# Performance work log

Measured on AMD Instinct MI355X. Metric: run time of the kernel, lower is better.

The kernel has to match this reference:

```python
import jax, jax.numpy as jnp
import numpy as np

B, P, T = 4096, 16, 8
IN_DIM, OUT_DIM, K = 128, 128, 2
N_TABLE = 100000


def setup_inputs() -> dict:
    key = jax.random.key(0)
    ks = jax.random.split(key, 8)
    return {
        "path_input": jax.random.randint(ks[0], (B, P, T), 0, N_TABLE, dtype=jnp.int32),
        "path_num": P,
        "timestamp": T,
        "path_type": jax.random.randint(ks[1], (T,), 0, 4, dtype=jnp.int32),
        "user_emb": jax.random.normal(ks[2], (N_TABLE, IN_DIM), jnp.float32),
        "item_emb": jax.random.normal(ks[3], (N_TABLE, IN_DIM), jnp.float32),
        "ca_emb": jax.random.normal(ks[4], (N_TABLE, IN_DIM), jnp.float32),
        "ci_emb": jax.random.normal(ks[5], (N_TABLE, IN_DIM), jnp.float32),
        "conv_w": jax.random.normal(ks[6], (OUT_DIM, IN_DIM, K), jnp.float32) * 0.05,
        "conv_b": jax.random.normal(ks[7], (OUT_DIM,), jnp.float32) * 0.05,
    }


def reference(path_input, path_num, timestamp, path_type,
              user_emb, item_emb, ca_emb, ci_emb, conv_w, conv_b):
    b, p, t = path_input.shape
    # [4, N, D] stacked tables; per-position table selection via path_type
    tables = jnp.stack([user_emb, item_emb, ca_emb, ci_emb])
    # emb: [B, P, T, D]  (advanced indexing: path_type broadcasts over B, P)
    emb = tables[path_type[None, None, :], path_input]
    # conv1d over time: [B*P, D, T] -> [B*P, out, T-K+1]
    x = emb.reshape(b * p, t, -1).transpose(0, 2, 1)
    y = jax.lax.conv_general_dilated(
        x, conv_w, window_strides=(1,), padding='VALID',
        dimension_numbers=('NCH', 'OIH', 'NCH')) + conv_b[None, :, None]
    # max-pool over time, then over paths (dropout is identity in eval)
    y = y.max(axis=-1).reshape(b, p, -1)  # [B, P, out]
    return y.max(axis=1)  # [B, out]
```

## Files before the change

### kernel.cpp

```cpp
#include <hip/hip_runtime.h>

#define NB   4096
#define NBLK 256
#define NJ   16

typedef __attribute__((ext_vector_type(4))) float f32x4;
typedef __attribute__((ext_vector_type(8))) short short8;
typedef __attribute__((ext_vector_type(4))) int   int4v;
typedef __attribute__((ext_vector_type(2))) int   int2v;

union Frag { int4v i; short8 s; };

__device__ __forceinline__ unsigned short f2bf(float f) {
  unsigned int u = __float_as_uint(f);
  u = (u + 0x7FFFu + ((u >> 16) & 1u)) >> 16;
  return (unsigned short)u;
}

__device__ __forceinline__ int cvtpk(float lo, float hi) {
  int r;
  asm("v_cvt_pk_bf16_f32 %0, %1, %2" : "=v"(r) : "v"(lo), "v"(hi));
  return r;
}

__global__ __launch_bounds__(512)
void wconv_kernel(const float* __restrict__ conv_w, unsigned short* __restrict__ ws)
{
  int flat = blockIdx.x * 512 + threadIdx.x;
  int lane = flat & 63;
  int ng   = (flat >> 6) & 7;
  int ker  = (flat >> 9) & 1;
  int kk   = flat >> 10;
  int col  = ng * 16 + (lane & 15);
  int k0   = kk * 32 + (lane >> 4) * 8;
  short8 s;
#pragma unroll
  for (int j = 0; j < 8; ++j)
    s[j] = (short)f2bf(conv_w[col * 256 + (k0 + j) * 2 + ker]);
  *(short8*)(ws + (size_t)flat * 8) = s;
}

#define RED_OFF 35088
#define LDS_BYTES 36112
#define A_STRIDE 272

__global__ __launch_bounds__(512)
void path_emb_kernel(const int* __restrict__ path_input,
                     const int* __restrict__ path_type,
                     const float* __restrict__ t0, const float* __restrict__ t1,
                     const float* __restrict__ t2, const float* __restrict__ t3,
                     const unsigned short* __restrict__ wfrag,
                     const float* __restrict__ conv_b,
                     float* __restrict__ out)
{
  __shared__ __align__(16) char lds[LDS_BYTES];
  const int blk  = blockIdx.x;
  const int tid  = threadIdx.x;
  const int wid  = tid >> 6;
  const int lane = tid & 63;
  const int lrow = lane & 15;
  const int lk   = lane >> 4;
  const int R = wid & 1;
  const int C = wid >> 1;

  const int* idxg = path_input + (size_t)blk * NJ * 128;
  float cb = (tid < 128) ? conv_b[tid] : 0.0f;

  const int grow = tid >> 2;
  const int gq   = tid & 3;
  const int ty   = path_type[grow & 7];
  const float* tb = (ty == 0) ? t0 : (ty == 1) ? t1 : (ty == 2) ? t2 : t3;

  Frag wreg[4][2][2];
#pragma unroll
  for (int kk = 0; kk < 4; ++kk)
#pragma unroll
    for (int ker = 0; ker < 2; ++ker)
#pragma unroll
      for (int n = 0; n < 2; ++n) {
        int f = (kk * 2 + ker) * 8 + C * 2 + n;
        wreg[kk][ker][n].i = *(const int4v*)(wfrag + (size_t)f * 512 + lane * 8);
      }

  auto ISSUE = [&](int j, f32x4 (&ld)[8]) {
    int idx = idxg[j * 128 + grow];
    const float* g = tb + (size_t)idx * 128 + gq * 4;
#pragma unroll
    for (int i = 0; i < 8; ++i) ld[i] = *(const f32x4*)(g + i * 16);
  };
  auto WRITE = [&](const f32x4 (&ld)[8]) {
    char* dst = lds + grow * A_STRIDE + gq * 8;
#pragma unroll
    for (int i = 0; i < 8; ++i) {
      int2v w;
      w[0] = cvtpk(ld[i][0], ld[i][1]);
      w[1] = cvtpk(ld[i][2], ld[i][3]);
      *(int2v*)(dst + i * 32) = w;
    }
  };

  float* red = (float*)(lds + RED_OFF);
  const int arow0 = R * 64 + lrow;

  auto COMPUTE = [&]() {
    f32x4 acc[4][2] = {};
#pragma unroll
    for (int kk = 0; kk < 4; ++kk) {
      Frag alo[4], ahi[4];
#pragma unroll
      for (int m = 0; m < 4; ++m) {
        const char* p = lds + (arow0 + m * 16) * A_STRIDE + kk * 64 + lk * 16;
        alo[m].i = *(const int4v*)(p);
        ahi[m].i = *(const int4v*)(p + A_STRIDE);
      }
#pragma unroll
      for (int m = 0; m < 4; ++m)
#pragma unroll
        for (int n = 0; n < 2; ++n) {
          acc[m][n] = __builtin_amdgcn_mfma_f32_16x16x32_bf16(
              alo[m].s, wreg[kk][0][n].s, acc[m][n], 0, 0, 0);
          acc[m][n] = __builtin_amdgcn_mfma_f32_16x16x32_bf16(
              ahi[m].s, wreg[kk][1][n].s, acc[m][n], 0, 0, 0);
        }
    }
    float vmax[2] = {-1e30f, -1e30f};
#pragma unroll
    for (int m = 0; m < 4; ++m)
#pragma unroll
      for (int n = 0; n < 2; ++n)
#pragma unroll
        for (int r = 0; r < 4; ++r) {
          int rloc = lk * 4 + r;
          if ((rloc & 7) == 7) continue;
          vmax[n] = fmaxf(vmax[n], acc[m][n][r]);
        }
#pragma unroll
    for (int n = 0; n < 2; ++n) {
      float v = vmax[n];
      v = fmaxf(v, __shfl_xor(v, 16));
      v = fmaxf(v, __shfl_xor(v, 32));
      vmax[n] = v;
    }
    if (lane < 16) {
#pragma unroll
      for (int n = 0; n < 2; ++n)
        red[R * 128 + C * 32 + n * 16 + lane] = vmax[n];
    }
  };

  auto BAR = [&]() {
    asm volatile("s_waitcnt lgkmcnt(0)" ::: "memory");
    __builtin_amdgcn_sched_barrier(0);
    __builtin_amdgcn_s_barrier();
    __builtin_amdgcn_sched_barrier(0);
  };

  f32x4 lA[8], lB[8], lC[8];
  ISSUE(0, lA);
  ISSUE(1, lB);
  ISSUE(2, lC);
  WRITE(lA);
  BAR();

#pragma unroll
  for (int j = 0; j < NJ; ++j) {
    if (j + 3 < NJ) {
      if (j % 3 == 0)      ISSUE(j + 3, lA);
      else if (j % 3 == 1) ISSUE(j + 3, lB);
      else                 ISSUE(j + 3, lC);
    }
    __builtin_amdgcn_sched_barrier(0);

    COMPUTE();
    BAR();

    if (tid < 128)
      out[(size_t)(blk * NJ + j) * 128 + tid] =
          fmaxf(red[tid], red[128 + tid]) + cb;

    if (j + 1 < NJ) {
      if ((j + 1) % 3 == 0)      WRITE(lA);
      else if ((j + 1) % 3 == 1) WRITE(lB);
      else                       WRITE(lC);
    }
    BAR();
  }
}

extern "C" void kernel_launch(void* const* d_in, const int* in_sizes, int n_in,
                              void* d_out, int out_size, void* d_ws, size_t ws_size,
                              hipStream_t stream) {
  const int*   path_input = (const int*)d_in[0];
  const int*   path_type  = (const int*)d_in[3];
  const float* user_emb   = (const float*)d_in[4];
  const float* item_emb   = (const float*)d_in[5];
  const float* ca_emb     = (const float*)d_in[6];
  const float* ci_emb     = (const float*)d_in[7];
  const float* conv_w     = (const float*)d_in[8];
  const float* conv_b     = (const float*)d_in[9];
  float* out = (float*)d_out;
  unsigned short* wfrag = (unsigned short*)d_ws;

  wconv_kernel<<<dim3(8), dim3(512), 0, stream>>>(conv_w, wfrag);
  path_emb_kernel<<<dim3(NBLK), dim3(512), 0, stream>>>(
      path_input, path_type, user_emb, item_emb, ca_emb, ci_emb,
      wfrag, conv_b, out);
}
```

Baseline: 53.89 us.

## Split work into many small blocks with double-buffered LDS and no cross-wave reduction

```diff
diff --git a/kernel.cpp b/kernel.cpp
--- a/kernel.cpp
+++ b/kernel.cpp
@@ -1,8 +1,6 @@
 #include <hip/hip_runtime.h>
 
-#define NB   4096
-#define NBLK 256
-#define NJ   16
+#define NBLK 2048
 
 typedef __attribute__((ext_vector_type(4))) float f32x4;
 typedef __attribute__((ext_vector_type(8))) short short8;
@@ -40,11 +38,11 @@
   *(short8*)(ws + (size_t)flat * 8) = s;
 }
 
-#define RED_OFF 35088
-#define LDS_BYTES 36112
 #define A_STRIDE 272
+#define ABUF     (65 * A_STRIDE)
+#define LDS_BYTES (2 * ABUF)
 
-__global__ __launch_bounds__(512)
+__global__ __launch_bounds__(256)
 void path_emb_kernel(const int* __restrict__ path_input,
                      const int* __restrict__ path_type,
                      const float* __restrict__ t0, const float* __restrict__ t1,
@@ -56,20 +54,26 @@
   __shared__ __align__(16) char lds[LDS_BYTES];
   const int blk  = blockIdx.x;
   const int tid  = threadIdx.x;
-  const int wid  = tid >> 6;
+  const int C    = tid >> 6;
   const int lane = tid & 63;
   const int lrow = lane & 15;
-  const int lk   = lane >> 4;
-  const int R = wid & 1;
-  const int C = wid >> 1;
-
-  const int* idxg = path_input + (size_t)blk * NJ * 128;
-  float cb = (tid < 128) ? conv_b[tid] : 0.0f;
+  const int g    = lane >> 4;
 
   const int grow = tid >> 2;
   const int gq   = tid & 3;
+  {
+  }
   const int ty   = path_type[grow & 7];
   const float* tb = (ty == 0) ? t0 : (ty == 1) ? t1 : (ty == 2) ? t2 : t3;
+
+  int idx[4];
+#pragma unroll
+  for (int jb = 0; jb < 4; ++jb)
+    idx[jb] = path_input[((size_t)blk * 2 + (jb >> 1)) * 128 + (jb & 1) * 64 + grow];
+
+  float cb[2];
+#pragma unroll
+  for (int n = 0; n < 2; ++n) cb[n] = conv_b[C * 32 + n * 16 + lrow];
 
   Frag wreg[4][2][2];
 #pragma unroll
@@ -82,14 +86,14 @@
         wreg[kk][ker][n].i = *(const int4v*)(wfrag + (size_t)f * 512 + lane * 8);
       }
 
-  auto ISSUE = [&](int j, f32x4 (&ld)[8]) {
-    int idx = idxg[j * 128 + grow];
-    const float* g = tb + (size_t)idx * 128 + gq * 4;
+  f32x4 ld[8];
+  auto ISSUE = [&](int jb) {
+    const float* base = tb + (size_t)idx[jb] * 128 + gq * 4;
 #pragma unroll
-    for (int i = 0; i < 8; ++i) ld[i] = *(const f32x4*)(g + i * 16);
+    for (int i = 0; i < 8; ++i) ld[i] = *(const f32x4*)(base + i * 16);
   };
-  auto WRITE = [&](const f32x4 (&ld)[8]) {
-    char* dst = lds + grow * A_STRIDE + gq * 8;
+  auto WRITE = [&](int buf) {
+    char* dst = lds + buf * ABUF + grow * A_STRIDE + gq * 8;
 #pragma unroll
     for (int i = 0; i < 8; ++i) {
       int2v w;
@@ -99,52 +103,32 @@
     }
   };
 
-  float* red = (float*)(lds + RED_OFF);
-  const int arow0 = R * 64 + lrow;
+  float vmax[2] = {-1e30f, -1e30f};
 
-  auto COMPUTE = [&]() {
-    f32x4 acc[4][2] = {};
+  auto COMPUTE = [&](int buf) {
+    const char* Ab = lds + buf * ABUF;
 #pragma unroll
-    for (int kk = 0; kk < 4; ++kk) {
-      Frag alo[4], ahi[4];
+    for (int m = 0; m < 4; ++m) {
+      f32x4 acc[2] = {};
 #pragma unroll
-      for (int m = 0; m < 4; ++m) {
-        const char* p = lds + (arow0 + m * 16) * A_STRIDE + kk * 64 + lk * 16;
-        alo[m].i = *(const int4v*)(p);
-        ahi[m].i = *(const int4v*)(p + A_STRIDE);
+      for (int kk = 0; kk < 4; ++kk) {
+        Frag alo, ahi;
+        const char* p = Ab + (m * 16 + lrow) * A_STRIDE + kk * 64 + g * 16;
+        alo.i = *(const int4v*)(p);
+        ahi.i = *(const int4v*)(p + A_STRIDE);
+        acc[0] = __builtin_amdgcn_mfma_f32_16x16x32_bf16(alo.s, wreg[kk][0][0].s, acc[0], 0, 0, 0);
+        acc[1] = __builtin_amdgcn_mfma_f32_16x16x32_bf16(alo.s, wreg[kk][0][1].s, acc[1], 0, 0, 0);
+        acc[0] = __builtin_amdgcn_mfma_f32_16x16x32_bf16(ahi.s, wreg[kk][1][0].s, acc[0], 0, 0, 0);
+        acc[1] = __builtin_amdgcn_mfma_f32_16x16x32_bf16(ahi.s, wreg[kk][1][1].s, acc[1], 0, 0, 0);
       }
-#pragma unroll
-      for (int m = 0; m < 4; ++m)
-#pragma unroll
-        for (int n = 0; n < 2; ++n) {
-          acc[m][n] = __builtin_amdgcn_mfma_f32_16x16x32_bf16(
-              alo[m].s, wreg[kk][0][n].s, acc[m][n], 0, 0, 0);
-          acc[m][n] = __builtin_amdgcn_mfma_f32_16x16x32_bf16(
-              ahi[m].s, wreg[kk][1][n].s, acc[m][n], 0, 0, 0);
-        }
-    }
-    float vmax[2] = {-1e30f, -1e30f};
-#pragma unroll
-    for (int m = 0; m < 4; ++m)
 #pragma unroll
       for (int n = 0; n < 2; ++n)
 #pragma unroll
         for (int r = 0; r < 4; ++r) {
-          int rloc = lk * 4 + r;
+          int rloc = g * 4 + r;
           if ((rloc & 7) == 7) continue;
-          vmax[n] = fmaxf(vmax[n], acc[m][n][r]);
+          vmax[n] = fmaxf(vmax[n], acc[n][r]);
         }
-#pragma unroll
-    for (int n = 0; n < 2; ++n) {
-      float v = vmax[n];
-      v = fmaxf(v, __shfl_xor(v, 16));
-      v = fmaxf(v, __shfl_xor(v, 32));
-      vmax[n] = v;
-    }
-    if (lane < 16) {
-#pragma unroll
-      for (int n = 0; n < 2; ++n)
-        red[R * 128 + C * 32 + n * 16 + lane] = vmax[n];
     }
   };
 
@@ -155,34 +139,35 @@
     __builtin_amdgcn_sched_barrier(0);
   };
 
-  f32x4 lA[8], lB[8], lC[8];
-  ISSUE(0, lA);
-  ISSUE(1, lB);
-  ISSUE(2, lC);
-  WRITE(lA);
+  ISSUE(0);
+  WRITE(0);
   BAR();
 
 #pragma unroll
-  for (int j = 0; j < NJ; ++j) {
-    if (j + 3 < NJ) {
-      if (j % 3 == 0)      ISSUE(j + 3, lA);
-      else if (j % 3 == 1) ISSUE(j + 3, lB);
-      else                 ISSUE(j + 3, lC);
-    }
+  for (int jb = 0; jb < 4; ++jb) {
+    if (jb + 1 < 4) ISSUE(jb + 1);
     __builtin_amdgcn_sched_barrier(0);
 
-    COMPUTE();
-    BAR();
+    COMPUTE(jb & 1);
 
-    if (tid < 128)
-      out[(size_t)(blk * NJ + j) * 128 + tid] =
-          fmaxf(red[tid], red[128 + tid]) + cb;
+    if (jb & 1) {
+#pragma unroll
+      for (int n = 0; n < 2; ++n) {
+        float v = vmax[n];
+        v = fmaxf(v, __shfl_xor(v, 16));
+        v = fmaxf(v, __shfl_xor(v, 32));
+        vmax[n] = v;
+      }
+      if (lane < 16) {
+        int b = blk * 2 + (jb >> 1);
+#pragma unroll
+        for (int n = 0; n < 2; ++n)
+          out[(size_t)b * 128 + C * 32 + n * 16 + lrow] = vmax[n] + cb[n];
+      }
+      vmax[0] = -1e30f; vmax[1] = -1e30f;
+    }
 
-    if (j + 1 < NJ) {
-      if ((j + 1) % 3 == 0)      WRITE(lA);
-      else if ((j + 1) % 3 == 1) WRITE(lB);
-      else                       WRITE(lC);
-    }
+    if (jb + 1 < 4) WRITE((jb + 1) & 1);
     BAR();
   }
 }
@@ -202,7 +187,7 @@
   unsigned short* wfrag = (unsigned short*)d_ws;
 
   wconv_kernel<<<dim3(8), dim3(512), 0, stream>>>(conv_w, wfrag);
-  path_emb_kernel<<<dim3(NBLK), dim3(512), 0, stream>>>(
+  path_emb_kernel<<<dim3(NBLK), dim3(256), 0, stream>>>(
       path_input, path_type, user_emb, item_emb, ca_emb, ci_emb,
       wfrag, conv_b, out);
 }
```

New measurement: 50.95 us. 1.06x faster.
